# Kernel tuning notes

Measured on AMD Instinct MI355X. Metric: run time of the kernel, lower is better.

## Reference

```python
import jax, jax.numpy as jnp
import numpy as np

N = 100000   # nodes
F = 256      # in_dim
D = 128      # out_dim
K = 2        # hops (K+1 adjacency matrices)
E = 1600000  # edges per hop (avg degree 16)


def setup_inputs() -> dict:
    key = jax.random.key(0)
    ks = jax.random.split(key, 8)
    node_features = jax.random.normal(ks[0], (N, F), dtype=jnp.float32)
    edge_rows = jax.random.randint(ks[1], (K + 1, E), 0, N, dtype=jnp.int32)
    edge_cols = jax.random.randint(ks[2], (K + 1, E), 0, N, dtype=jnp.int32)
    edge_vals = jax.random.uniform(ks[3], (K + 1, E), dtype=jnp.float32)
    W_embed = jax.random.normal(ks[4], (F, D), dtype=jnp.float32) / np.sqrt(F)
    W_feat = jax.random.normal(ks[5], (K + 1, F, D), dtype=jnp.float32) / np.sqrt(F)
    W_embK = jax.random.normal(ks[6], (K + 1, D, D), dtype=jnp.float32) / np.sqrt(D)
    alpha = jnp.asarray(0.1, dtype=jnp.float32)  # learnable scalar, clipped to [0,1]
    return {
        'node_features': node_features,
        'edge_rows': edge_rows,
        'edge_cols': edge_cols,
        'edge_vals': edge_vals,
        'W_embed': W_embed,
        'W_feat': W_feat,
        'W_embK': W_embK,
        'alpha': alpha,
    }


def reference(node_features, edge_rows, edge_cols, edge_vals, W_embed, W_feat, W_embK, alpha):
    # learned_embeddings = Dense(out_dim, no bias)(X)  -> [N, D]
    learned = node_features @ W_embed
    out = jnp.zeros((node_features.shape[0], W_embed.shape[1]), dtype=node_features.dtype)
    for hop in range(K + 1):
        # feature projection for this hop: [N, D]
        fw = node_features @ W_feat[hop]
        # SpMM: A_hop @ fw via COO gather + scatter-add
        msgs = edge_vals[hop][:, None] * fw[edge_cols[hop]]            # [E, D]
        structural = jax.ops.segment_sum(msgs, edge_rows[hop], num_segments=node_features.shape[0])
        learned_h = learned @ W_embK[hop]                              # [N, D]
        out = out + structural + alpha * learned_h
    # dropout is identity at inference (training=False)
    return jax.nn.relu(out)
```

## Files before the change

### kernel.cpp

```cpp
#include <hip/hip_runtime.h>
#include <hip/hip_bf16.h>

#define F_DIM 256
#define D_DIM 128
#define NHOPS 3
#define KPB   256
#define NBMAX 2048

using short8 = __attribute__((ext_vector_type(8))) short;
using f32x4  = __attribute__((ext_vector_type(4))) float;

static __device__ __forceinline__ unsigned short f2bf(float f) {
    unsigned int u = __float_as_uint(f);
    unsigned int r = (u + 0x7fffu + ((u >> 16) & 1u)) >> 16;
    return (unsigned short)r;
}
static __device__ __forceinline__ float bf2f(unsigned short b) {
    return __uint_as_float(((unsigned int)b) << 16);
}
static __device__ __forceinline__ int2 ldnt_i2(const int2* p) {
    long long raw = __builtin_nontemporal_load((const long long*)p);
    int2 r; r.x = (int)(raw & 0xffffffffLL); r.y = (int)(raw >> 32);
    return r;
}

__global__ void wsum_kernel(const float* __restrict__ W_embK,
                            const float* __restrict__ alpha,
                            float* __restrict__ Wsum) {
    int i = blockIdx.x * blockDim.x + threadIdx.x;
    if (i < D_DIM * D_DIM) {
        float a = alpha[0];
        Wsum[i] = a * (W_embK[i] + W_embK[D_DIM * D_DIM + i] + W_embK[2 * D_DIM * D_DIM + i]);
    }
}

__global__ __launch_bounds__(256) void pack_all(const float* __restrict__ W_embed,
                                                const float* __restrict__ W_feat,
                                                const float* __restrict__ Wsum,
                                                unsigned short* __restrict__ Wt) {
    __shared__ float wcol[D_DIM];
    const int j = blockIdx.x;
    const int k = threadIdx.x;
    if (j < D_DIM) {
        for (int i = k; i < D_DIM; i += 256) wcol[i] = Wsum[i * D_DIM + j];
        __syncthreads();
        float acc = 0.f;
        #pragma unroll 8
        for (int kk = 0; kk < D_DIM; ++kk)
            acc = fmaf(W_embed[k * D_DIM + kk], wcol[kk], acc);
        Wt[(size_t)j * F_DIM + k] = f2bf(acc);
    } else {
        int hp = (j - D_DIM) >> 7, d = (j - D_DIM) & 127;
        Wt[(size_t)j * F_DIM + k] = f2bf(W_feat[(size_t)hp * F_DIM * D_DIM + k * D_DIM + d]);
    }
}

__global__ void xcast_kernel(const float* __restrict__ X, unsigned short* __restrict__ Xb,
                             int n4) {
    int i = blockIdx.x * blockDim.x + threadIdx.x;
    int stride = gridDim.x * blockDim.x;
    for (; i < n4; i += stride) {
        float4 v = ((const float4*)X)[i];
        ushort4 p;
        p.x = f2bf(v.x); p.y = f2bf(v.y); p.z = f2bf(v.z); p.w = f2bf(v.w);
        ((ushort4*)Xb)[i] = p;
    }
}


__global__ __launch_bounds__(256) void bhist_kernel(const int* __restrict__ rows,
                                                    int* __restrict__ bcount,
                                                    int N, int E, int TE) {
    __shared__ int h[NBMAX];
    int tid = threadIdx.x;
    for (int i = tid; i < NBMAX; i += 256) h[i] = 0;
    __syncthreads();
    int c0 = blockIdx.x * 4096;
    #pragma unroll
    for (int i = 0; i < 16; ++i) {
        int ge = c0 + tid + i * 256;
        if (ge < TE) {
            int row = rows[ge];
            int hp = (ge >= E) + (ge >= 2 * E);
            atomicAdd(&h[(hp * N + row) >> 8], 1);
        }
    }
    __syncthreads();
    for (int b = tid; b < NBMAX; b += 256)
        if (h[b]) atomicAdd(&bcount[b], h[b]);
}

__global__ __launch_bounds__(256) void bscan_kernel(const int* __restrict__ bcount,
                                                    int* __restrict__ bstart,
                                                    int* __restrict__ gcur, int NB) {
    __shared__ int s[256];
    int tid = threadIdx.x;
    int carry = 0;
    for (int base = 0; base < NB; base += 256) {
        int idx = base + tid;
        int v = (idx < NB) ? bcount[idx] : 0;
        s[tid] = v; __syncthreads();
        for (int off = 1; off < 256; off <<= 1) {
            int t = (tid >= off) ? s[tid - off] : 0;
            __syncthreads();
            s[tid] += t;
            __syncthreads();
        }
        int excl = carry + s[tid] - v;
        if (idx < NB) { bstart[idx] = excl; gcur[idx] = excl; }
        carry += s[255];
        __syncthreads();
    }
    if (tid == 0) bstart[NB] = carry;
}

__global__ __launch_bounds__(256) void bucket_scatter(const int* __restrict__ rows,
                                                      const int* __restrict__ cols,
                                                      const float* __restrict__ vals,
                                                      int* __restrict__ gcur,
                                                      int2* __restrict__ cvb,
                                                      int N, int E, int TE) {
    __shared__ int sh_hist[NBMAX];
    __shared__ int sh_gof[NBMAX];
    int tid = threadIdx.x;
    for (int i = tid; i < NBMAX; i += 256) sh_hist[i] = 0;
    __syncthreads();
    int c0 = blockIdx.x * 4096;
    unsigned meta[16];
    #pragma unroll
    for (int i = 0; i < 16; ++i) {
        int ge = c0 + tid + i * 256;
        unsigned m = 0;
        if (ge < TE) {
            int row = rows[ge];
            int hp = (ge >= E) + (ge >= 2 * E);
            int key = hp * N + row;
            int b = key >> 8;
            int lkey = key & 255;
            int rank = atomicAdd(&sh_hist[b], 1);
            m = ((unsigned)lkey << 23) | ((unsigned)b << 12) | (unsigned)rank;
        }
        meta[i] = m;
    }
    __syncthreads();
    for (int b = tid; b < NBMAX; b += 256)
        if (sh_hist[b]) sh_gof[b] = atomicAdd(&gcur[b], sh_hist[b]);
    __syncthreads();
    #pragma unroll
    for (int i = 0; i < 16; ++i) {
        int ge = c0 + tid + i * 256;
        if (ge < TE) {
            unsigned m = meta[i];
            int rank = m & 4095;
            int b = (m >> 12) & 2047;
            int lkey = m >> 23;
            cvb[sh_gof[b] + rank] = make_int2(cols[ge] | (lkey << 17),
                                              __float_as_int(vals[ge]));
        }
    }
}

__global__ __launch_bounds__(256) void local_sort(const int2* __restrict__ cvb,
                                                  const int* __restrict__ bstart,
                                                  int2* __restrict__ cv,
                                                  int* __restrict__ offsets,
                                                  int M, int TE, int NB) {
    __shared__ int h[256];
    __shared__ int sc[256];
    const int tid = threadIdx.x;
    const int b = blockIdx.x;
    const int s = bstart[b], e = bstart[b + 1];

    h[tid] = 0;
    __syncthreads();
    for (int i = s + tid; i < e; i += 256)
        atomicAdd(&h[((unsigned)cvb[i].x) >> 17], 1);
    __syncthreads();
    int v = h[tid];
    sc[tid] = v; __syncthreads();
    for (int off = 1; off < 256; off <<= 1) {
        int t = (tid >= off) ? sc[tid - off] : 0;
        __syncthreads();
        sc[tid] += t;
        __syncthreads();
    }
    int excl = sc[tid] - v;
    int key = (b << 8) + tid;
    if (key < M) offsets[key] = s + excl;
    if (b == NB - 1 && tid == 0) offsets[M] = TE;
    h[tid] = excl;
    __syncthreads();
    for (int i = s + tid; i < e; i += 256) {
        int2 rec = cvb[i];
        unsigned lkey = ((unsigned)rec.x) >> 17;
        int p = s + atomicAdd(&h[lkey], 1);
        cv[p] = make_int2(rec.x & 0x1FFFF, rec.y);
    }
}


__global__ void hist_kernel(const int* __restrict__ rows, int* __restrict__ counts,
                            int N, int E) {
    int idx = blockIdx.x * blockDim.x + threadIdx.x;
    int h = blockIdx.y;
    if (idx < E) atomicAdd(&counts[h * N + rows[(size_t)h * E + idx]], 1);
}

__global__ void scan1(const int* __restrict__ counts, int* __restrict__ tmp,
                      int* __restrict__ bsums, int M) {
    __shared__ int s[256];
    int tid = threadIdx.x, i = blockIdx.x * 256 + tid;
    int v = (i < M) ? counts[i] : 0;
    s[tid] = v; __syncthreads();
    for (int off = 1; off < 256; off <<= 1) {
        int t = (tid >= off) ? s[tid - off] : 0;
        __syncthreads();
        s[tid] += t;
        __syncthreads();
    }
    if (i < M) tmp[i] = s[tid] - v;
    if (tid == 255) bsums[blockIdx.x] = s[255];
}

__global__ void scan2(int* __restrict__ bsums, int nb) {
    __shared__ int s[256];
    int tid = threadIdx.x;
    int carry = 0;
    for (int base = 0; base < nb; base += 256) {
        int v = (base + tid < nb) ? bsums[base + tid] : 0;
        s[tid] = v; __syncthreads();
        for (int off = 1; off < 256; off <<= 1) {
            int t = (tid >= off) ? s[tid - off] : 0;
            __syncthreads();
            s[tid] += t;
            __syncthreads();
        }
        if (base + tid < nb) bsums[base + tid] = carry + s[tid] - v;
        carry += s[255];
        __syncthreads();
    }
}

__global__ void scan3(int* __restrict__ tmp, const int* __restrict__ bsums,
                      int* __restrict__ offsets, int M, int total) {
    int i = blockIdx.x * blockDim.x + threadIdx.x;
    if (i < M) {
        int e = tmp[i] + bsums[i >> 8];
        offsets[i] = e;
        tmp[i] = e;
    }
    if (i == 0) offsets[M] = total;
}

__global__ void scatter_kernel(const int* __restrict__ rows, const int* __restrict__ cols,
                               const float* __restrict__ vals, int* __restrict__ cursors,
                               int2* __restrict__ cv, int N, int E) {
    int idx = blockIdx.x * blockDim.x + threadIdx.x;
    int h = blockIdx.y;
    if (idx < E) {
        size_t e = (size_t)h * E + idx;
        int r = rows[e];
        int p = atomicAdd(&cursors[h * N + r], 1);
        cv[p] = make_int2(cols[e], __float_as_int(vals[e]));
    }
}

template <bool BF16A>
__global__ __launch_bounds__(256) void gemm_mfma(const float* __restrict__ X,
                                                 const unsigned short* __restrict__ Xb,
                                                 const unsigned short* __restrict__ Wt,
                                                 float* __restrict__ out,
                                                 unsigned short* __restrict__ fw,
                                                 int N) {
    __shared__ __align__(16) unsigned short As[128][40];
    __shared__ __align__(16) unsigned short Bs[128][40];

    const int tid = threadIdx.x;
    const int w = tid >> 6, lane = tid & 63;
    const int bm = blockIdx.x, bn = blockIdx.y;
    const int row0 = bm * 128;
    const int wm = (w & 1) * 64, wn = (w >> 1) * 64;
    const int l15 = lane & 15, lk = (lane >> 4) * 8;

    f32x4 acc[4][4] = {};

    for (int k0 = 0; k0 < F_DIM; k0 += 32) {
        float4 bv[2];
        #pragma unroll
        for (int i = 0; i < 2; ++i) {
            int idx = tid + i * 256;
            int br = idx >> 2, kq = (idx & 3) << 3;
            bv[i] = *(const float4*)&Wt[((size_t)(bn * 128 + br)) * F_DIM + k0 + kq];
        }
        if constexpr (BF16A) {
            short8 av[2];
            #pragma unroll
            for (int i = 0; i < 2; ++i) {
                int idx = tid + i * 256;
                int ar = idx >> 2, kq = (idx & 3) << 3;
                int gr = row0 + ar; if (gr >= N) gr = N - 1;
                av[i] = *(const short8*)&Xb[(size_t)gr * F_DIM + k0 + kq];
            }
            __syncthreads();
            #pragma unroll
            for (int i = 0; i < 2; ++i) {
                int idx = tid + i * 256;
                int ar = idx >> 2, kq = (idx & 3) << 3;
                *(short8*)&As[ar][kq] = av[i];
            }
        } else {
            float4 av[4];
            #pragma unroll
            for (int i = 0; i < 4; ++i) {
                int idx = tid + i * 256;
                int ar = idx >> 3, kq = (idx & 7) << 2;
                int gr = row0 + ar; if (gr >= N) gr = N - 1;
                av[i] = *(const float4*)&X[(size_t)gr * F_DIM + k0 + kq];
            }
            __syncthreads();
            #pragma unroll
            for (int i = 0; i < 4; ++i) {
                int idx = tid + i * 256;
                int ar = idx >> 3, kq = (idx & 7) << 2;
                ushort4 p;
                p.x = f2bf(av[i].x); p.y = f2bf(av[i].y);
                p.z = f2bf(av[i].z); p.w = f2bf(av[i].w);
                *(ushort4*)&As[ar][kq] = p;
            }
        }
        #pragma unroll
        for (int i = 0; i < 2; ++i) {
            int idx = tid + i * 256;
            int br = idx >> 2, kq = (idx & 3) << 3;
            *(float4*)&Bs[br][kq] = bv[i];
        }
        __syncthreads();

        short8 af[4], bfr[4];
        #pragma unroll
        for (int mi = 0; mi < 4; ++mi) af[mi]  = *(const short8*)&As[wm + mi * 16 + l15][lk];
        #pragma unroll
        for (int ni = 0; ni < 4; ++ni) bfr[ni] = *(const short8*)&Bs[wn + ni * 16 + l15][lk];
        #pragma unroll
        for (int mi = 0; mi < 4; ++mi)
            #pragma unroll
            for (int ni = 0; ni < 4; ++ni)
                acc[mi][ni] = __builtin_amdgcn_mfma_f32_16x16x32_bf16(af[mi], bfr[ni], acc[mi][ni], 0, 0, 0);
        __syncthreads();
    }

    if (bn == 0) {
        #pragma unroll
        for (int mi = 0; mi < 4; ++mi) {
            int rowb = row0 + wm + mi * 16 + (lane >> 4) * 4;
            #pragma unroll
            for (int ni = 0; ni < 4; ++ni) {
                int col = wn + ni * 16 + l15;
                #pragma unroll
                for (int j = 0; j < 4; ++j) {
                    int rr = rowb + j;
                    if (rr < N) out[(size_t)rr * D_DIM + col] = acc[mi][ni][j];
                }
            }
        }
    } else {
        unsigned short* dst = fw + (size_t)(bn - 1) * N * D_DIM;
        #pragma unroll
        for (int mi = 0; mi < 4; ++mi) {
            int rowb = row0 + wm + mi * 16 + (lane >> 4) * 4;
            #pragma unroll
            for (int ni = 0; ni < 4; ++ni) {
                int col = wn + ni * 16 + l15;
                #pragma unroll
                for (int j = 0; j < 4; ++j) {
                    int rr = rowb + j;
                    if (rr < N) dst[(size_t)rr * D_DIM + col] = f2bf(acc[mi][ni][j]);
                }
            }
        }
    }
}

__global__ __launch_bounds__(256) void spmm_csr(const int* __restrict__ off,
                                                const int2* __restrict__ cv,
                                                const unsigned short* __restrict__ fw,
                                                float* __restrict__ out, int N) {
    const int w = threadIdx.x >> 6, lane = threadIdx.x & 63;
    const int r = blockIdx.x * 4 + w;
    if (r >= N) return;
    const int sub = lane >> 4;
    const int dp  = lane & 15;
    const size_t obase = (size_t)r * D_DIM + dp * 8;

    float acc[8];
    if (sub == 0) {
        float4 a = *(const float4*)&out[obase];
        float4 b = *(const float4*)&out[obase + 4];
        acc[0] = a.x; acc[1] = a.y; acc[2] = a.z; acc[3] = a.w;
        acc[4] = b.x; acc[5] = b.y; acc[6] = b.z; acc[7] = b.w;
    } else {
        #pragma unroll
        for (int j = 0; j < 8; ++j) acc[j] = 0.f;
    }

    #pragma unroll
    for (int h = 0; h < NHOPS; ++h) {
        const unsigned short* fwh = fw + (size_t)h * N * D_DIM;
        int s = off[h * N + r], e = off[h * N + r + 1];
        int i = s + sub;
        for (; i + 12 < e; i += 16) {
            int2 c0 = ldnt_i2(cv + i);
            int2 c1 = ldnt_i2(cv + i + 4);
            int2 c2 = ldnt_i2(cv + i + 8);
            int2 c3 = ldnt_i2(cv + i + 12);
            short8 p0 = *(const short8*)&fwh[(size_t)c0.x * D_DIM + dp * 8];
            short8 p1 = *(const short8*)&fwh[(size_t)c1.x * D_DIM + dp * 8];
            short8 p2 = *(const short8*)&fwh[(size_t)c2.x * D_DIM + dp * 8];
            short8 p3 = *(const short8*)&fwh[(size_t)c3.x * D_DIM + dp * 8];
            float v0 = __int_as_float(c0.y), v1 = __int_as_float(c1.y);
            float v2 = __int_as_float(c2.y), v3 = __int_as_float(c3.y);
            #pragma unroll
            for (int j = 0; j < 8; ++j) acc[j] = fmaf(v0, bf2f((unsigned short)p0[j]), acc[j]);
            #pragma unroll
            for (int j = 0; j < 8; ++j) acc[j] = fmaf(v1, bf2f((unsigned short)p1[j]), acc[j]);
            #pragma unroll
            for (int j = 0; j < 8; ++j) acc[j] = fmaf(v2, bf2f((unsigned short)p2[j]), acc[j]);
            #pragma unroll
            for (int j = 0; j < 8; ++j) acc[j] = fmaf(v3, bf2f((unsigned short)p3[j]), acc[j]);
        }
        for (; i + 4 < e; i += 8) {
            int2 c0 = ldnt_i2(cv + i);
            int2 c1 = ldnt_i2(cv + i + 4);
            short8 p0 = *(const short8*)&fwh[(size_t)c0.x * D_DIM + dp * 8];
            short8 p1 = *(const short8*)&fwh[(size_t)c1.x * D_DIM + dp * 8];
            float v0 = __int_as_float(c0.y), v1 = __int_as_float(c1.y);
            #pragma unroll
            for (int j = 0; j < 8; ++j) acc[j] = fmaf(v0, bf2f((unsigned short)p0[j]), acc[j]);
            #pragma unroll
            for (int j = 0; j < 8; ++j) acc[j] = fmaf(v1, bf2f((unsigned short)p1[j]), acc[j]);
        }
        if (i < e) {
            int2 c0 = ldnt_i2(cv + i);
            short8 p0 = *(const short8*)&fwh[(size_t)c0.x * D_DIM + dp * 8];
            float v0 = __int_as_float(c0.y);
            #pragma unroll
            for (int j = 0; j < 8; ++j) acc[j] = fmaf(v0, bf2f((unsigned short)p0[j]), acc[j]);
        }
    }

    #pragma unroll
    for (int j = 0; j < 8; ++j) {
        acc[j] += __shfl_xor(acc[j], 16, 64);
        acc[j] += __shfl_xor(acc[j], 32, 64);
    }

    if (sub == 0) {
        float4 a = {fmaxf(acc[0], 0.f), fmaxf(acc[1], 0.f), fmaxf(acc[2], 0.f), fmaxf(acc[3], 0.f)};
        float4 b = {fmaxf(acc[4], 0.f), fmaxf(acc[5], 0.f), fmaxf(acc[6], 0.f), fmaxf(acc[7], 0.f)};
        *(float4*)&out[obase]     = a;
        *(float4*)&out[obase + 4] = b;
    }
}

extern "C" void kernel_launch(void* const* d_in, const int* in_sizes, int n_in,
                              void* d_out, int out_size, void* d_ws, size_t ws_size,
                              hipStream_t stream) {
    const float* X         = (const float*)d_in[0];
    const int*   edge_rows = (const int*)d_in[1];
    const int*   edge_cols = (const int*)d_in[2];
    const float* edge_vals = (const float*)d_in[3];
    const float* W_embed   = (const float*)d_in[4];
    const float* W_feat    = (const float*)d_in[5];
    const float* W_embK    = (const float*)d_in[6];
    const float* alpha     = (const float*)d_in[7];
    float* out = (float*)d_out;

    const int N  = in_sizes[0] / F_DIM;
    const int E  = in_sizes[1] / NHOPS;
    const int M  = NHOPS * N;
    const int TE = NHOPS * E;
    const int NB = (M + KPB - 1) / KPB;

    auto al = [](size_t x) { return (x + 255) & ~(size_t)255; };
    const size_t sz_cv  = al((size_t)TE * 8);
    const size_t sz_fwb = al((size_t)M * D_DIM * 2);
    const size_t sz_xb  = al((size_t)N * F_DIM * 2);
    const size_t sz_off = al((size_t)(M + 1) * 4);
    const size_t sz_b   = al((size_t)(NBMAX + 1) * 4);
    const size_t sz_w   = al(D_DIM * D_DIM * 4) + al(512 * F_DIM * 2);
    const size_t need_mid = 2 * sz_cv + sz_fwb + sz_off + 3 * sz_b + sz_w;
    const size_t need_big = need_mid + sz_xb;

    const bool ok_new = (NB <= NBMAX) && (N < (1 << 17));
    const int mode = (ok_new && ws_size >= need_big) ? 2
                   : (ok_new && ws_size >= need_mid) ? 1 : 0;

    char* wsb = (char*)d_ws;
    size_t o = 0;
    auto take = [&](size_t bytes) -> char* {
        char* p = wsb + o;
        o += al(bytes);
        return p;
    };

    if (mode >= 1) {
        int2*           cvb     = (int2*)take((size_t)TE * 8);
        int2*           cv      = (int2*)take((size_t)TE * 8);
        unsigned short* fwb     = (unsigned short*)take((size_t)M * D_DIM * 2);
        int*            offsets = (int*)take((size_t)(M + 1) * 4);
        int*            bcount  = (int*)take((NBMAX + 1) * 4);
        int*            bstart  = (int*)take((NBMAX + 1) * 4);
        int*            gcur    = (int*)take((NBMAX + 1) * 4);
        float*          Wsum    = (float*)take(D_DIM * D_DIM * 4);
        unsigned short* Wt      = (unsigned short*)take(512 * F_DIM * 2);
        unsigned short* Xb      = (mode == 2) ? (unsigned short*)take((size_t)N * F_DIM * 2) : nullptr;

        const int nchunk = (TE + 4095) / 4096;
        hipMemsetAsync(bcount, 0, NBMAX * 4, stream);
        bhist_kernel<<<nchunk, 256, 0, stream>>>(edge_rows, bcount, N, E, TE);
        bscan_kernel<<<1, 256, 0, stream>>>(bcount, bstart, gcur, NB);
        bucket_scatter<<<nchunk, 256, 0, stream>>>(edge_rows, edge_cols, edge_vals,
                                                   gcur, cvb, N, E, TE);
        local_sort<<<NB, 256, 0, stream>>>(cvb, bstart, cv, offsets, M, TE, NB);

        wsum_kernel<<<(D_DIM * D_DIM + 255) / 256, 256, 0, stream>>>(W_embK, alpha, Wsum);
        pack_all<<<512, 256, 0, stream>>>(W_embed, W_feat, Wsum, Wt);

        dim3 g((N + 127) / 128, 4);
        if (mode == 2) {
            xcast_kernel<<<2048, 256, 0, stream>>>(X, Xb, N * F_DIM / 4);
            gemm_mfma<true><<<g, 256, 0, stream>>>(X, Xb, Wt, out, fwb, N);
        } else {
            gemm_mfma<false><<<g, 256, 0, stream>>>(X, nullptr, Wt, out, fwb, N);
        }

        spmm_csr<<<(N + 3) / 4, 256, 0, stream>>>(offsets, cv, fwb, out, N);
    } else {
        int2*           cv      = (int2*)take((size_t)TE * 8);
        unsigned short* fwb     = (unsigned short*)take((size_t)M * D_DIM * 2);
        int*            counts  = (int*)take((size_t)M * 4);
        int*            cursors = (int*)take((size_t)M * 4);
        int*            offsets = (int*)take((size_t)(M + 1) * 4);
        int*            bsums   = (int*)take(8192);
        float*          Wsum    = (float*)take(D_DIM * D_DIM * 4);
        unsigned short* Wt      = (unsigned short*)take(512 * F_DIM * 2);

        hipMemsetAsync(counts, 0, (size_t)M * 4, stream);
        dim3 ge((E + 255) / 256, NHOPS);
        hist_kernel<<<ge, 256, 0, stream>>>(edge_rows, counts, N, E);
        int nb = (M + 255) / 256;
        scan1<<<nb, 256, 0, stream>>>(counts, cursors, bsums, M);
        scan2<<<1, 256, 0, stream>>>(bsums, nb);
        scan3<<<nb, 256, 0, stream>>>(cursors, bsums, offsets, M, TE);
        scatter_kernel<<<ge, 256, 0, stream>>>(edge_rows, edge_cols, edge_vals,
                                               cursors, cv, N, E);

        wsum_kernel<<<(D_DIM * D_DIM + 255) / 256, 256, 0, stream>>>(W_embK, alpha, Wsum);
        pack_all<<<512, 256, 0, stream>>>(W_embed, W_feat, Wsum, Wt);

        dim3 g((N + 127) / 128, 4);
        gemm_mfma<false><<<g, 256, 0, stream>>>(X, nullptr, Wt, out, fwb, N);

        spmm_csr<<<(N + 3) / 4, 256, 0, stream>>>(offsets, cv, fwb, out, N);
    }
}
```

Measured before the change: 675.4 us.

## Restructure GEMM to stage full X tile once, widen sort buckets, fuse weight prep

The GEMM now loads and converts each 128-row X tile to bf16 in LDS once and loops over all four output column blocks, replacing the separate xcast pass and four-fold X reads. The bucket sort uses 1024-key buckets with 8192-edge chunks, giving fewer buckets and larger local sorts. The Wsum kernel is folded into pack_all, and the SpMM drops its 16-wide unrolled nontemporal loop for a simpler 8-wide loop with normal loads. The risks are lower occupancy from the larger LDS footprint in the GEMM and less memory-level parallelism in the SpMM.

```diff
diff --git a/kernel.cpp b/kernel.cpp
--- a/kernel.cpp
+++ b/kernel.cpp
@@ -4,8 +4,9 @@
 #define F_DIM 256
 #define D_DIM 128
 #define NHOPS 3
-#define KPB   256
-#define NBMAX 2048
+#define KPB   1024
+#define NBMAX 640
+#define CHUNK 8192
 
 using short8 = __attribute__((ext_vector_type(8))) short;
 using f32x4  = __attribute__((ext_vector_type(4))) float;
@@ -18,31 +19,21 @@
 static __device__ __forceinline__ float bf2f(unsigned short b) {
     return __uint_as_float(((unsigned int)b) << 16);
 }
-static __device__ __forceinline__ int2 ldnt_i2(const int2* p) {
-    long long raw = __builtin_nontemporal_load((const long long*)p);
-    int2 r; r.x = (int)(raw & 0xffffffffLL); r.y = (int)(raw >> 32);
-    return r;
-}
-
-__global__ void wsum_kernel(const float* __restrict__ W_embK,
-                            const float* __restrict__ alpha,
-                            float* __restrict__ Wsum) {
-    int i = blockIdx.x * blockDim.x + threadIdx.x;
-    if (i < D_DIM * D_DIM) {
-        float a = alpha[0];
-        Wsum[i] = a * (W_embK[i] + W_embK[D_DIM * D_DIM + i] + W_embK[2 * D_DIM * D_DIM + i]);
-    }
-}
 
 __global__ __launch_bounds__(256) void pack_all(const float* __restrict__ W_embed,
                                                 const float* __restrict__ W_feat,
-                                                const float* __restrict__ Wsum,
+                                                const float* __restrict__ W_embK,
+                                                const float* __restrict__ alpha,
                                                 unsigned short* __restrict__ Wt) {
     __shared__ float wcol[D_DIM];
     const int j = blockIdx.x;
     const int k = threadIdx.x;
     if (j < D_DIM) {
-        for (int i = k; i < D_DIM; i += 256) wcol[i] = Wsum[i * D_DIM + j];
+        float a = alpha[0];
+        for (int i = k; i < D_DIM; i += 256)
+            wcol[i] = a * (W_embK[i * D_DIM + j] +
+                           W_embK[D_DIM * D_DIM + i * D_DIM + j] +
+                           W_embK[2 * D_DIM * D_DIM + i * D_DIM + j]);
         __syncthreads();
         float acc = 0.f;
         #pragma unroll 8
@@ -55,18 +46,6 @@
     }
 }
 
-__global__ void xcast_kernel(const float* __restrict__ X, unsigned short* __restrict__ Xb,
-                             int n4) {
-    int i = blockIdx.x * blockDim.x + threadIdx.x;
-    int stride = gridDim.x * blockDim.x;
-    for (; i < n4; i += stride) {
-        float4 v = ((const float4*)X)[i];
-        ushort4 p;
-        p.x = f2bf(v.x); p.y = f2bf(v.y); p.z = f2bf(v.z); p.w = f2bf(v.w);
-        ((ushort4*)Xb)[i] = p;
-    }
-}
-
 
 __global__ __launch_bounds__(256) void bhist_kernel(const int* __restrict__ rows,
                                                     int* __restrict__ bcount,
@@ -75,14 +54,14 @@
     int tid = threadIdx.x;
     for (int i = tid; i < NBMAX; i += 256) h[i] = 0;
     __syncthreads();
-    int c0 = blockIdx.x * 4096;
-    #pragma unroll
-    for (int i = 0; i < 16; ++i) {
+    int c0 = blockIdx.x * CHUNK;
+    #pragma unroll 4
+    for (int i = 0; i < CHUNK / 256; ++i) {
         int ge = c0 + tid + i * 256;
         if (ge < TE) {
             int row = rows[ge];
             int hp = (ge >= E) + (ge >= 2 * E);
-            atomicAdd(&h[(hp * N + row) >> 8], 1);
+            atomicAdd(&h[(hp * N + row) >> 10], 1);
         }
     }
     __syncthreads();
@@ -125,20 +104,18 @@
     int tid = threadIdx.x;
     for (int i = tid; i < NBMAX; i += 256) sh_hist[i] = 0;
     __syncthreads();
-    int c0 = blockIdx.x * 4096;
-    unsigned meta[16];
-    #pragma unroll
-    for (int i = 0; i < 16; ++i) {
+    int c0 = blockIdx.x * CHUNK;
+    unsigned meta[CHUNK / 256];
+    #pragma unroll 4
+    for (int i = 0; i < CHUNK / 256; ++i) {
         int ge = c0 + tid + i * 256;
-        unsigned m = 0;
+        unsigned m = 0xFFFFFFFFu;
         if (ge < TE) {
             int row = rows[ge];
             int hp = (ge >= E) + (ge >= 2 * E);
-            int key = hp * N + row;
-            int b = key >> 8;
-            int lkey = key & 255;
-            int rank = atomicAdd(&sh_hist[b], 1);
-            m = ((unsigned)lkey << 23) | ((unsigned)b << 12) | (unsigned)rank;
+            unsigned key = (unsigned)(hp * N + row);
+            int rank = atomicAdd(&sh_hist[key >> 10], 1);
+            m = (key << 13) | (unsigned)rank;
         }
         meta[i] = m;
     }
@@ -146,14 +123,15 @@
     for (int b = tid; b < NBMAX; b += 256)
         if (sh_hist[b]) sh_gof[b] = atomicAdd(&gcur[b], sh_hist[b]);
     __syncthreads();
-    #pragma unroll
-    for (int i = 0; i < 16; ++i) {
+    #pragma unroll 4
+    for (int i = 0; i < CHUNK / 256; ++i) {
         int ge = c0 + tid + i * 256;
         if (ge < TE) {
             unsigned m = meta[i];
-            int rank = m & 4095;
-            int b = (m >> 12) & 2047;
-            int lkey = m >> 23;
+            int rank = m & 8191;
+            unsigned key = m >> 13;
+            int b = key >> 10;
+            int lkey = key & 1023;
             cvb[sh_gof[b] + rank] = make_int2(cols[ge] | (lkey << 17),
                                               __float_as_int(vals[ge]));
         }
@@ -165,30 +143,38 @@
                                                   int2* __restrict__ cv,
                                                   int* __restrict__ offsets,
                                                   int M, int TE, int NB) {
-    __shared__ int h[256];
-    __shared__ int sc[256];
+    __shared__ int h[KPB];
+    __shared__ int part[256];
     const int tid = threadIdx.x;
     const int b = blockIdx.x;
     const int s = bstart[b], e = bstart[b + 1];
 
-    h[tid] = 0;
+    for (int k = tid; k < KPB; k += 256) h[k] = 0;
     __syncthreads();
     for (int i = s + tid; i < e; i += 256)
         atomicAdd(&h[((unsigned)cvb[i].x) >> 17], 1);
     __syncthreads();
-    int v = h[tid];
-    sc[tid] = v; __syncthreads();
+    int base4 = tid * 4;
+    int a0 = h[base4], a1 = h[base4 + 1], a2 = h[base4 + 2], a3 = h[base4 + 3];
+    part[tid] = a0 + a1 + a2 + a3;
+    __syncthreads();
     for (int off = 1; off < 256; off <<= 1) {
-        int t = (tid >= off) ? sc[tid - off] : 0;
-        __syncthreads();
-        sc[tid] += t;
-        __syncthreads();
-    }
-    int excl = sc[tid] - v;
-    int key = (b << 8) + tid;
-    if (key < M) offsets[key] = s + excl;
+        int t = (tid >= off) ? part[tid - off] : 0;
+        __syncthreads();
+        part[tid] += t;
+        __syncthreads();
+    }
+    int pbase = tid ? part[tid - 1] : 0;
+    h[base4]     = pbase;
+    h[base4 + 1] = pbase + a0;
+    h[base4 + 2] = pbase + a0 + a1;
+    h[base4 + 3] = pbase + a0 + a1 + a2;
+    __syncthreads();
+    for (int k = tid; k < KPB; k += 256) {
+        int key = (b << 10) + k;
+        if (key < M) offsets[key] = s + h[k];
+    }
     if (b == NB - 1 && tid == 0) offsets[M] = TE;
-    h[tid] = excl;
     __syncthreads();
     for (int i = s + tid; i < e; i += 256) {
         int2 rec = cvb[i];
@@ -265,116 +251,92 @@
     }
 }
 
-template <bool BF16A>
 __global__ __launch_bounds__(256) void gemm_mfma(const float* __restrict__ X,
-                                                 const unsigned short* __restrict__ Xb,
                                                  const unsigned short* __restrict__ Wt,
                                                  float* __restrict__ out,
                                                  unsigned short* __restrict__ fw,
                                                  int N) {
-    __shared__ __align__(16) unsigned short As[128][40];
+    __shared__ __align__(16) unsigned short As[128][F_DIM + 8];
     __shared__ __align__(16) unsigned short Bs[128][40];
 
     const int tid = threadIdx.x;
     const int w = tid >> 6, lane = tid & 63;
-    const int bm = blockIdx.x, bn = blockIdx.y;
-    const int row0 = bm * 128;
+    const int row0 = blockIdx.x * 128;
     const int wm = (w & 1) * 64, wn = (w >> 1) * 64;
     const int l15 = lane & 15, lk = (lane >> 4) * 8;
 
-    f32x4 acc[4][4] = {};
-
-    for (int k0 = 0; k0 < F_DIM; k0 += 32) {
-        float4 bv[2];
-        #pragma unroll
-        for (int i = 0; i < 2; ++i) {
-            int idx = tid + i * 256;
-            int br = idx >> 2, kq = (idx & 3) << 3;
-            bv[i] = *(const float4*)&Wt[((size_t)(bn * 128 + br)) * F_DIM + k0 + kq];
-        }
-        if constexpr (BF16A) {
-            short8 av[2];
+    #pragma unroll
+    for (int i = 0; i < 32; ++i) {
+        int idx = tid + i * 256;
+        int ar = idx >> 6;
+        int kq = (idx & 63) << 2;
+        int gr = row0 + ar; if (gr >= N) gr = N - 1;
+        float4 v = *(const float4*)&X[(size_t)gr * F_DIM + kq];
+        ushort4 p;
+        p.x = f2bf(v.x); p.y = f2bf(v.y); p.z = f2bf(v.z); p.w = f2bf(v.w);
+        *(ushort4*)&As[ar][kq] = p;
+    }
+
+    for (int bn = 0; bn < 4; ++bn) {
+        f32x4 acc[4][4] = {};
+        for (int k0 = 0; k0 < F_DIM; k0 += 32) {
+            float4 bv[2];
             #pragma unroll
             for (int i = 0; i < 2; ++i) {
                 int idx = tid + i * 256;
-                int ar = idx >> 2, kq = (idx & 3) << 3;
-                int gr = row0 + ar; if (gr >= N) gr = N - 1;
-                av[i] = *(const short8*)&Xb[(size_t)gr * F_DIM + k0 + kq];
+                int br = idx >> 2, kq = (idx & 3) << 3;
+                bv[i] = *(const float4*)&Wt[((size_t)(bn * 128 + br)) * F_DIM + k0 + kq];
             }
             __syncthreads();
             #pragma unroll
             for (int i = 0; i < 2; ++i) {
                 int idx = tid + i * 256;
-                int ar = idx >> 2, kq = (idx & 3) << 3;
-                *(short8*)&As[ar][kq] = av[i];
+                int br = idx >> 2, kq = (idx & 3) << 3;
+                *(float4*)&Bs[br][kq] = bv[i];
+            }
+            __syncthreads();
+
+            short8 af[4], bfr[4];
+            #pragma unroll
+            for (int mi = 0; mi < 4; ++mi)
+                af[mi] = *(const short8*)&As[wm + mi * 16 + l15][k0 + lk];
+            #pragma unroll
+            for (int ni = 0; ni < 4; ++ni)
+                bfr[ni] = *(const short8*)&Bs[wn + ni * 16 + l15][lk];
+            #pragma unroll
+            for (int mi = 0; mi < 4; ++mi)
+                #pragma unroll
+                for (int ni = 0; ni < 4; ++ni)
+                    acc[mi][ni] = __builtin_amdgcn_mfma_f32_16x16x32_bf16(af[mi], bfr[ni], acc[mi][ni], 0, 0, 0);
+        }
+
+        if (bn == 0) {
+            #pragma unroll
+            for (int mi = 0; mi < 4; ++mi) {
+                int rowb = row0 + wm + mi * 16 + (lane >> 4) * 4;
+                #pragma unroll
+                for (int ni = 0; ni < 4; ++ni) {
+                    int col = wn + ni * 16 + l15;
+                    #pragma unroll
+                    for (int j = 0; j < 4; ++j) {
+                        int rr = rowb + j;
+                        if (rr < N) out[(size_t)rr * D_DIM + col] = acc[mi][ni][j];
+                    }
+                }
             }
         } else {
-            float4 av[4];
-            #pragma unroll
-            for (int i = 0; i < 4; ++i) {
-                int idx = tid + i * 256;
-                int ar = idx >> 3, kq = (idx & 7) << 2;
-                int gr = row0 + ar; if (gr >= N) gr = N - 1;
-                av[i] = *(const float4*)&X[(size_t)gr * F_DIM + k0 + kq];
-            }
-            __syncthreads();
-            #pragma unroll
-            for (int i = 0; i < 4; ++i) {
-                int idx = tid + i * 256;
-                int ar = idx >> 3, kq = (idx & 7) << 2;
-                ushort4 p;
-                p.x = f2bf(av[i].x); p.y = f2bf(av[i].y);
-                p.z = f2bf(av[i].z); p.w = f2bf(av[i].w);
-                *(ushort4*)&As[ar][kq] = p;
-            }
-        }
-        #pragma unroll
-        for (int i = 0; i < 2; ++i) {
-            int idx = tid + i * 256;
-            int br = idx >> 2, kq = (idx & 3) << 3;
-            *(float4*)&Bs[br][kq] = bv[i];
-        }
-        __syncthreads();
-
-        short8 af[4], bfr[4];
-        #pragma unroll
-        for (int mi = 0; mi < 4; ++mi) af[mi]  = *(const short8*)&As[wm + mi * 16 + l15][lk];
-        #pragma unroll
-        for (int ni = 0; ni < 4; ++ni) bfr[ni] = *(const short8*)&Bs[wn + ni * 16 + l15][lk];
-        #pragma unroll
-        for (int mi = 0; mi < 4; ++mi)
-            #pragma unroll
-            for (int ni = 0; ni < 4; ++ni)
-                acc[mi][ni] = __builtin_amdgcn_mfma_f32_16x16x32_bf16(af[mi], bfr[ni], acc[mi][ni], 0, 0, 0);
-        __syncthreads();
-    }
-
-    if (bn == 0) {
-        #pragma unroll
-        for (int mi = 0; mi < 4; ++mi) {
-            int rowb = row0 + wm + mi * 16 + (lane >> 4) * 4;
-            #pragma unroll
-            for (int ni = 0; ni < 4; ++ni) {
-                int col = wn + ni * 16 + l15;
+            unsigned short* dst = fw + (size_t)(bn - 1) * N * D_DIM;
+            #pragma unroll
+            for (int mi = 0; mi < 4; ++mi) {
+                int rowb = row0 + wm + mi * 16 + (lane >> 4) * 4;
                 #pragma unroll
-                for (int j = 0; j < 4; ++j) {
-                    int rr = rowb + j;
-                    if (rr < N) out[(size_t)rr * D_DIM + col] = acc[mi][ni][j];
-                }
-            }
-        }
-    } else {
-        unsigned short* dst = fw + (size_t)(bn - 1) * N * D_DIM;
-        #pragma unroll
-        for (int mi = 0; mi < 4; ++mi) {
-            int rowb = row0 + wm + mi * 16 + (lane >> 4) * 4;
-            #pragma unroll
-            for (int ni = 0; ni < 4; ++ni) {
-                int col = wn + ni * 16 + l15;
-                #pragma unroll
-                for (int j = 0; j < 4; ++j) {
-                    int rr = rowb + j;
-                    if (rr < N) dst[(size_t)rr * D_DIM + col] = f2bf(acc[mi][ni][j]);
+                for (int ni = 0; ni < 4; ++ni) {
+                    int col = wn + ni * 16 + l15;
+                    #pragma unroll
+                    for (int j = 0; j < 4; ++j) {
+                        int rr = rowb + j;
+                        if (rr < N) dst[(size_t)rr * D_DIM + col] = f2bf(acc[mi][ni][j]);
+                    }
                 }
             }
         }
@@ -408,43 +370,27 @@
         const unsigned short* fwh = fw + (size_t)h * N * D_DIM;
         int s = off[h * N + r], e = off[h * N + r + 1];
         int i = s + sub;
-        for (; i + 12 < e; i += 16) {
-            int2 c0 = ldnt_i2(cv + i);
-            int2 c1 = ldnt_i2(cv + i + 4);
-            int2 c2 = ldnt_i2(cv + i + 8);
-            int2 c3 = ldnt_i2(cv + i + 12);
-            short8 p0 = *(const short8*)&fwh[(size_t)c0.x * D_DIM + dp * 8];
-            short8 p1 = *(const short8*)&fwh[(size_t)c1.x * D_DIM + dp * 8];
-            short8 p2 = *(const short8*)&fwh[(size_t)c2.x * D_DIM + dp * 8];
-            short8 p3 = *(const short8*)&fwh[(size_t)c3.x * D_DIM + dp * 8];
-            float v0 = __int_as_float(c0.y), v1 = __int_as_float(c1.y);
-            float v2 = __int_as_float(c2.y), v3 = __int_as_float(c3.y);
-            #pragma unroll
-            for (int j = 0; j < 8; ++j) acc[j] = fmaf(v0, bf2f((unsigned short)p0[j]), acc[j]);
-            #pragma unroll
-            for (int j = 0; j < 8; ++j) acc[j] = fmaf(v1, bf2f((unsigned short)p1[j]), acc[j]);
-            #pragma unroll
-            for (int j = 0; j < 8; ++j) acc[j] = fmaf(v2, bf2f((unsigned short)p2[j]), acc[j]);
-            #pragma unroll
-            for (int j = 0; j < 8; ++j) acc[j] = fmaf(v3, bf2f((unsigned short)p3[j]), acc[j]);
-        }
         for (; i + 4 < e; i += 8) {
-            int2 c0 = ldnt_i2(cv + i);
-            int2 c1 = ldnt_i2(cv + i + 4);
-            short8 p0 = *(const short8*)&fwh[(size_t)c0.x * D_DIM + dp * 8];
-            short8 p1 = *(const short8*)&fwh[(size_t)c1.x * D_DIM + dp * 8];
-            float v0 = __int_as_float(c0.y), v1 = __int_as_float(c1.y);
-            #pragma unroll
-            for (int j = 0; j < 8; ++j) acc[j] = fmaf(v0, bf2f((unsigned short)p0[j]), acc[j]);
-            #pragma unroll
-            for (int j = 0; j < 8; ++j) acc[j] = fmaf(v1, bf2f((unsigned short)p1[j]), acc[j]);
+            int2 ca = cv[i];
+            int2 cb = cv[i + 4];
+            short8 pa = *(const short8*)&fwh[(size_t)ca.x * D_DIM + dp * 8];
+            short8 pb = *(const short8*)&fwh[(size_t)cb.x * D_DIM + dp * 8];
+            float va = __int_as_float(ca.y);
+            float vb = __int_as_float(cb.y);
+            #pragma unroll
+            for (int j = 0; j < 8; ++j)
+                acc[j] = fmaf(va, bf2f((unsigned short)pa[j]), acc[j]);
+            #pragma unroll
+            for (int j = 0; j < 8; ++j)
+                acc[j] = fmaf(vb, bf2f((unsigned short)pb[j]), acc[j]);
         }
         if (i < e) {
-            int2 c0 = ldnt_i2(cv + i);
-            short8 p0 = *(const short8*)&fwh[(size_t)c0.x * D_DIM + dp * 8];
-            float v0 = __int_as_float(c0.y);
-            #pragma unroll
-            for (int j = 0; j < 8; ++j) acc[j] = fmaf(v0, bf2f((unsigned short)p0[j]), acc[j]);
+            int2 ca = cv[i];
+            short8 pa = *(const short8*)&fwh[(size_t)ca.x * D_DIM + dp * 8];
+            float va = __int_as_float(ca.y);
+            #pragma unroll
+            for (int j = 0; j < 8; ++j)
+                acc[j] = fmaf(va, bf2f((unsigned short)pa[j]), acc[j]);
         }
     }
 
@@ -484,16 +430,12 @@
     auto al = [](size_t x) { return (x + 255) & ~(size_t)255; };
     const size_t sz_cv  = al((size_t)TE * 8);
     const size_t sz_fwb = al((size_t)M * D_DIM * 2);
-    const size_t sz_xb  = al((size_t)N * F_DIM * 2);
     const size_t sz_off = al((size_t)(M + 1) * 4);
     const size_t sz_b   = al((size_t)(NBMAX + 1) * 4);
-    const size_t sz_w   = al(D_DIM * D_DIM * 4) + al(512 * F_DIM * 2);
-    const size_t need_mid = 2 * sz_cv + sz_fwb + sz_off + 3 * sz_b + sz_w;
-    const size_t need_big = need_mid + sz_xb;
-
-    const bool ok_new = (NB <= NBMAX) && (N < (1 << 17));
-    const int mode = (ok_new && ws_size >= need_big) ? 2
-                   : (ok_new && ws_size >= need_mid) ? 1 : 0;
+    const size_t sz_wt  = al(512 * F_DIM * 2);
+    const size_t need_new = 2 * sz_cv + sz_fwb + sz_off + 3 * sz_b + sz_wt;
+
+    const bool ok_new = (NB <= NBMAX) && (N < (1 << 17)) && (ws_size >= need_new);
 
     char* wsb = (char*)d_ws;
     size_t o = 0;
@@ -503,7 +445,7 @@
         return p;
     };
 
-    if (mode >= 1) {
+    if (ok_new) {
         int2*           cvb     = (int2*)take((size_t)TE * 8);
         int2*           cv      = (int2*)take((size_t)TE * 8);
         unsigned short* fwb     = (unsigned short*)take((size_t)M * D_DIM * 2);
@@ -511,11 +453,9 @@
         int*            bcount  = (int*)take((NBMAX + 1) * 4);
         int*            bstart  = (int*)take((NBMAX + 1) * 4);
         int*            gcur    = (int*)take((NBMAX + 1) * 4);
-        float*          Wsum    = (float*)take(D_DIM * D_DIM * 4);
         unsigned short* Wt      = (unsigned short*)take(512 * F_DIM * 2);
-        unsigned short* Xb      = (mode == 2) ? (unsigned short*)take((size_t)N * F_DIM * 2) : nullptr;
-
-        const int nchunk = (TE + 4095) / 4096;
+
+        const int nchunk = (TE + CHUNK - 1) / CHUNK;
         hipMemsetAsync(bcount, 0, NBMAX * 4, stream);
         bhist_kernel<<<nchunk, 256, 0, stream>>>(edge_rows, bcount, N, E, TE);
         bscan_kernel<<<1, 256, 0, stream>>>(bcount, bstart, gcur, NB);
@@ -523,16 +463,9 @@
                                                    gcur, cvb, N, E, TE);
         local_sort<<<NB, 256, 0, stream>>>(cvb, bstart, cv, offsets, M, TE, NB);
 
-        wsum_kernel<<<(D_DIM * D_DIM + 255) / 256, 256, 0, stream>>>(W_embK, alpha, Wsum);
-        pack_all<<<512, 256, 0, stream>>>(W_embed, W_feat, Wsum, Wt);
-
-        dim3 g((N + 127) / 128, 4);
-        if (mode == 2) {
-            xcast_kernel<<<2048, 256, 0, stream>>>(X, Xb, N * F_DIM / 4);
-            gemm_mfma<true><<<g, 256, 0, stream>>>(X, Xb, Wt, out, fwb, N);
-        } else {
-            gemm_mfma<false><<<g, 256, 0, stream>>>(X, nullptr, Wt, out, fwb, N);
-        }
+        pack_all<<<512, 256, 0, stream>>>(W_embed, W_feat, W_embK, alpha, Wt);
+
+        gemm_mfma<<<(N + 127) / 128, 256, 0, stream>>>(X, Wt, out, fwb, N);
 
         spmm_csr<<<(N + 3) / 4, 256, 0, stream>>>(offsets, cv, fwb, out, N);
     } else {
@@ -542,7 +475,6 @@
         int*            cursors = (int*)take((size_t)M * 4);
         int*            offsets = (int*)take((size_t)(M + 1) * 4);
         int*            bsums   = (int*)take(8192);
-        float*          Wsum    = (float*)take(D_DIM * D_DIM * 4);
         unsigned short* Wt      = (unsigned short*)take(512 * F_DIM * 2);
 
         hipMemsetAsync(counts, 0, (size_t)M * 4, stream);
@@ -555,11 +487,9 @@
         scatter_kernel<<<ge, 256, 0, stream>>>(edge_rows, edge_cols, edge_vals,
                                                cursors, cv, N, E);
 
-        wsum_kernel<<<(D_DIM * D_DIM + 255) / 256, 256, 0, stream>>>(W_embK, alpha, Wsum);
-        pack_all<<<512, 256, 0, stream>>>(W_embed, W_feat, Wsum, Wt);
-
-        dim3 g((N + 127) / 128, 4);
-        gemm_mfma<false><<<g, 256, 0, stream>>>(X, nullptr, Wt, out, fwb, N);
+        pack_all<<<512, 256, 0, stream>>>(W_embed, W_feat, W_embK, alpha, Wt);
+
+        gemm_mfma<<<(N + 127) / 128, 256, 0, stream>>>(X, Wt, out, fwb, N);
 
         spmm_csr<<<(N + 3) / 4, 256, 0, stream>>>(offsets, cv, fwb, out, N);
     }
```

New measurement: 630.6 us. 1.07x faster.
